# Performance work log

Measured on AMD Instinct MI355X. Metric: run time of the kernel, lower is better.

The kernel has to match this reference:

```python
import jax, jax.numpy as jnp
from jax import lax
import numpy as np

EPS = 1e-5

def sign_ste(x):
    # Binarize to {-1,+1} with straight-through estimator (matches BNN Binarize)
    return x + lax.stop_gradient(jnp.where(x >= 0, 1.0, -1.0).astype(x.dtype) - x)

def bn(x, g, b, m, v, axis):
    shp = [1] * x.ndim
    shp[axis] = -1
    inv = g.reshape(shp) / jnp.sqrt(v.reshape(shp) + EPS)
    return (x - m.reshape(shp)) * inv + b.reshape(shp)

def bconv(x, w, b, p):
    # binarized-weight conv, NCHW / OIHW
    y = lax.conv_general_dilated(x, sign_ste(w), (1, 1), [(p, p), (p, p)],
                                 dimension_numbers=('NCHW', 'OIHW', 'NCHW'))
    return y + b[None, :, None, None]

def conv_block(x, w, b, g, bt, m, v, p):
    # BinarizeConv2d -> BatchNorm2d(eval) -> Hardtanh -> Quantizer(1 bit)
    return sign_ste(jnp.clip(bn(bconv(x, w, b, p), g, bt, m, v, 1), -1.0, 1.0))

def maxpool2(x):
    return lax.reduce_window(x, -jnp.inf, lax.max, (1, 1, 2, 2), (1, 1, 2, 2), 'VALID')


def setup_inputs() -> dict:
    key = jax.random.key(0)
    ks = iter(jax.random.split(key, 64))
    B = 4096
    d = {}
    d['x'] = jax.random.normal(next(ks), (B, 1, 28, 28), dtype=jnp.float32)

    def u(shape):
        return jax.random.uniform(next(ks), shape, minval=-1.0, maxval=1.0, dtype=jnp.float32)

    def bn_params(c, pre):
        d[pre + 'g'] = u((c,)) * 0.5 + 1.0
        d[pre + 'bt'] = u((c,)) * 0.1
        d[pre + 'm'] = u((c,)) * 0.1
        d[pre + 'v'] = jax.random.uniform(next(ks), (c,), minval=0.5, maxval=1.5, dtype=jnp.float32)

    # stem conv 1->16, k=3
    d['w1'] = u((16, 1, 3, 3)); d['b1'] = jnp.full((16,), 0.01, jnp.float32); bn_params(16, '')
    d['g1'], d['bt1'], d['m1'], d['v1'] = d.pop('g'), d.pop('bt'), d.pop('m'), d.pop('v')
    # inception branches 16->32 each
    d['wa'] = u((32, 16, 1, 1)); d['ba'] = jnp.full((32,), 0.01, jnp.float32); bn_params(32, 'a_')
    d['wb'] = u((32, 16, 3, 3)); d['bb'] = jnp.full((32,), 0.01, jnp.float32); bn_params(32, 'b_')
    d['wc'] = u((32, 16, 5, 5)); d['bc'] = jnp.full((32,), 0.01, jnp.float32); bn_params(32, 'c_')
    # classifier
    d['wf1'] = u((1024, 7 * 7 * 3 * 32)); d['bf1'] = jnp.full((1024,), 0.01, jnp.float32); bn_params(1024, 'f1_')
    d['wf2'] = u((10, 1024)); d['bf2'] = jnp.full((10,), 0.01, jnp.float32); bn_params(10, 'f2_')
    return d


def reference(x, w1, b1, g1, bt1, m1, v1,
              wa, ba, a_g, a_bt, a_m, a_v,
              wb, bb, b_g, b_bt, b_m, b_v,
              wc, bc, c_g, c_bt, c_m, c_v,
              wf1, bf1, f1_g, f1_bt, f1_m, f1_v,
              wf2, bf2, f2_g, f2_bt, f2_m, f2_v):
    h = conv_block(x, w1, b1, g1, bt1, m1, v1, 1)          # [B,16,28,28]
    h = maxpool2(h)                                         # [B,16,14,14]
    h = sign_ste(h)  # BinarizeConv2d binarizes its input (>1 channel); no-op on +/-1
    ya = conv_block(h, wa, ba, a_g, a_bt, a_m, a_v, 0)
    yb = conv_block(h, wb, bb, b_g, b_bt, b_m, b_v, 1)
    yc = conv_block(h, wc, bc, c_g, c_bt, c_m, c_v, 2)
    h = jnp.concatenate([ya, yb, yc], axis=1)               # [B,96,14,14]
    h = maxpool2(h)                                         # [B,96,7,7]
    h = h.reshape(h.shape[0], -1)                           # [B,4704] (NCHW flatten)
    # fc1: binarized input + binarized weights, BN1d, hardtanh, quantize
    h = sign_ste(h) @ sign_ste(wf1).T + bf1
    h = sign_ste(jnp.clip(bn(h, f1_g, f1_bt, f1_m, f1_v, 1), -1.0, 1.0))
    # dropout is identity in eval mode
    h = sign_ste(h) @ sign_ste(wf2).T + bf2
    h = bn(h, f2_g, f2_bt, f2_m, f2_v, 1)
    return jax.nn.log_softmax(h, axis=-1)                   # [B,10]
```

## Files before the change

### kernel.cpp

```cpp
#include <hip/hip_runtime.h>
#include <stdint.h>

typedef unsigned long long u64;
typedef unsigned int u32;
typedef unsigned short u16;

struct InPtrs { const float* p[37]; };

#define OFF_THR1     0
#define OFF_W1D      128
#define OFF_WREC     1280
#define OFF_SMAXBC   4352
#define OFF_SMAXF1   11008
#define OFF_WF2P     15104
#define OFF_A2       16384
#define OFF_C2       16448
#define OFF_WF1P     16512
#define OFF_H2       622720
#define OFF_HB2      3047552

__device__ __forceinline__ int clampi(int v, int lo, int hi) { return v < lo ? lo : (v > hi ? hi : v); }

__global__ __launch_bounds__(1024) void kprep(InPtrs P, char* __restrict__ ws) {
  const float* w1 = P.p[1]; const float* b1 = P.p[2];
  const float* g1 = P.p[3]; const float* bt1 = P.p[4]; const float* m1 = P.p[5]; const float* v1 = P.p[6];
  const float* wa = P.p[7]; const float* ba = P.p[8];
  const float* ag = P.p[9]; const float* abt = P.p[10]; const float* am = P.p[11]; const float* av = P.p[12];
  const float* wb = P.p[13]; const float* bb = P.p[14];
  const float* bg = P.p[15]; const float* bbt = P.p[16]; const float* bm = P.p[17]; const float* bv = P.p[18];
  const float* wc = P.p[19]; const float* bc = P.p[20];
  const float* bf1 = P.p[26];
  const float* f1g = P.p[27]; const float* f1bt = P.p[28]; const float* f1m = P.p[29]; const float* f1v = P.p[30];
  const float* wf2 = P.p[31]; const float* bf2 = P.p[32];
  const float* cg = P.p[21]; const float* cbt = P.p[22]; const float* cm = P.p[23]; const float* cv = P.p[24];
  const float* f2g = P.p[33]; const float* f2bt = P.p[34]; const float* f2m = P.p[35]; const float* f2v = P.p[36];

  double* thr1 = (double*)(ws + OFF_THR1);
  double* w1d  = (double*)(ws + OFF_W1D);
  u64* wrec = (u64*)(ws + OFF_WREC);
  u64* smaxbc = (u64*)(ws + OFF_SMAXBC);
  int* smf1 = (int*)(ws + OFF_SMAXF1);
  u64* wf2p = (u64*)(ws + OFF_WF2P);
  float* a2 = (float*)(ws + OFF_A2);
  float* c2 = (float*)(ws + OFF_C2);

  __shared__ u64 wbpL[96];
  __shared__ u64 wcpL[256];
  __shared__ double thBL[32], thCL[32];
  __shared__ u32 wamS[32], smaS[32];

  int t = threadIdx.x;
  int wave = t >> 6, lane = t & 63;

  if (t < 144) w1d[t] = (w1[t] >= 0.f) ? 1.0 : -1.0;
  if (t < 16) {
    double inv = (double)g1[t] / sqrt((double)v1[t] + 1e-5);
    thr1[t] = (double)m1[t] - (double)bt1[t] / inv - (double)b1[t];
  }
  if (t < 32) {
    u32 m = 0;
    for (int c = 0; c < 16; c++) if (wa[t*16+c] >= 0.f) m |= 1u << c;
    wamS[t] = m;
    double ia = (double)ag[t] / sqrt((double)av[t] + 1e-5);
    double thA = (double)am[t] - (double)abt[t]/ia - (double)ba[t];
    int kmin = (int)ceil(thA);
    int sm = (16 - kmin) >> 1;
    smaS[t] = (u32)clampi(sm + 1, 0, 65535);
    double ib = (double)bg[t] / sqrt((double)bv[t] + 1e-5);
    thBL[t] = (double)bm[t] - (double)bbt[t]/ib - (double)bb[t];
    double ic = (double)cg[t] / sqrt((double)cv[t] + 1e-5);
    thCL[t] = (double)cm[t] - (double)cbt[t]/ic - (double)bc[t];
  }
  for (int w = wave; w < 96; w += 16) {
    int ch = w / 3, k = w - 3*ch;
    int tt = 4*k + (lane >> 4), c = lane & 15;
    bool pred = false;
    if (tt < 9) pred = (wb[ch*144 + c*9 + tt] >= 0.f);
    u64 m = __ballot(pred);
    if (lane == 0) wbpL[w] = m;
  }
  for (int w = wave; w < 256; w += 16) {
    int ch = w >> 3, k = w & 7;
    int tt = 4*k + (lane >> 4), c = lane & 15;
    bool pred = false;
    if (k < 7 && tt < 25) pred = (wc[ch*400 + c*25 + tt] >= 0.f);
    u64 m = __ballot(pred);
    if (lane == 0) wcpL[w] = m;
  }
  for (int w = wave; w < 160; w += 16) {
    int o = w >> 4, kk = w & 15;
    bool pred = (wf2[o*1024 + kk*64 + lane] >= 0.f);
    u64 m = __ballot(pred);
    if (lane == 0) wf2p[w] = m;
  }
  if (t < 10) {
    double inv = (double)f2g[t] / sqrt((double)f2v[t] + 1e-5);
    a2[t] = (float)inv;
    c2[t] = (float)(((double)bf2[t] - (double)f2m[t]) * inv + (double)f2bt[t]);
  }
  {
    int o = t;
    double inv = (double)f1g[o] / sqrt((double)f1v[o] + 1e-5);
    double th = (double)f1m[o] - (double)f1bt[o]/inv - (double)bf1[o];
    int kmin = (int)ceil(th);
    smf1[o] = ((4704 - kmin) >> 1) + 1;
  }
  __syncthreads();
  if (t < 384) {
    int ch = t / 12, k = t - 12*ch;
    u64 v = 0;
    if (k < 7) v = wcpL[ch*8 + k];
    else if (k < 10) v = wbpL[ch*3 + (k - 7)];
    wrec[ch*12 + k] = v;
  }
  if (t < 800) {
    const int irep[5] = {0, 1, 5, 12, 13};
    int cls = t >> 5, ch = t & 31;
    int rc = cls / 5, cc = cls - 5*rc;
    int ir = irep[rc], jr = irep[cc];
    u64 invC[7] = {0,0,0,0,0,0,0};
    u64 invB[3] = {0,0,0};
    int nInvC = 0, nInvB = 0;
    #pragma unroll
    for (int tt = 0; tt < 25; tt++) {
      int di = tt/5 - 2, dj = tt%5 - 2;
      bool val = (ir+di >= 0 && ir+di < 14 && jr+dj >= 0 && jr+dj < 14);
      if (!val) { invC[tt>>2] |= 0xFFFFull << ((tt&3)*16); nInvC++; }
    }
    #pragma unroll
    for (int tt = 0; tt < 9; tt++) {
      int di = tt/3 - 1, dj = tt%3 - 1;
      bool val = (ir+di >= 0 && ir+di < 14 && jr+dj >= 0 && jr+dj < 14);
      if (!val) { invB[tt>>2] |= 0xFFFFull << ((tt&3)*16); nInvB++; }
    }
    int pinvC = 0;
    #pragma unroll
    for (int k = 0; k < 7; k++) pinvC += __popcll(wcpL[ch*8+k] & invC[k]);
    int pinvB = 0;
    #pragma unroll
    for (int k = 0; k < 3; k++) pinvB += __popcll(wbpL[ch*3+k] & invB[k]);
    int nvC = 16*(25 - nInvC), nvB = 16*(9 - nInvB);
    int kminC = (int)ceil(thCL[ch]);
    int kminB = (int)ceil(thBL[ch]);
    int smC = ((nvC - kminC) >> 1) + pinvC;
    int smB = ((nvB - kminB) >> 1) + pinvB;
    u64 pB = (u64)clampi(smB + 1, 0, 65535);
    u64 pC = (u64)clampi(smC + 1, 0, 65535);
    smaxbc[cls*33 + ch] = ((u64)wamS[ch] << 48) | ((u64)smaS[ch] << 32) | (pB << 16) | pC;
  }
}

__global__ __launch_bounds__(256) void kfused(const float* __restrict__ x, const float* __restrict__ wf1,
                                              const char* __restrict__ ws,
                                              u32* __restrict__ h2u32, u64* __restrict__ wf1p) {
  __shared__ float wshF[144];
  __shared__ float thrF[16];
  __shared__ double thrD[16];
  __shared__ u16 hp[324];
  __shared__ u32 rr[196][3];
  __shared__ u64 smbc[825];
  __shared__ __align__(16) u64 wrecL[384];

  int t = threadIdx.x;

  if (blockIdx.x < 1024) {
    unsigned char* flag = (unsigned char*)smbc;
    int o = blockIdx.x;
    const float* row = wf1 + (size_t)o*4704;
    for (int i = t; i < 4704; i += 256) flag[i] = (row[i] >= 0.f);
    __syncthreads();
    int w0 = t >> 6, lane = t & 63;
    for (int w = w0; w < 74; w += 4) {
      int fp = w*64 + lane;
      bool bit = false;
      if (fp < 4704) { int s = fp / 96, c = fp - 96*s; bit = flag[c*49 + s] != 0; }
      u64 m = __ballot(bit);
      if (lane == 0) wf1p[(size_t)o*74 + w] = m;
    }
    return;
  }

  int b = blockIdx.x - 1024;
  const double* w1d  = (const double*)(ws + OFF_W1D);
  const double* thr1 = (const double*)(ws + OFF_THR1);
  const u64* wrec_g = (const u64*)(ws + OFF_WREC);
  const u64* smaxbc_g = (const u64*)(ws + OFF_SMAXBC);

  if (t < 144) wshF[t] = (float)w1d[t];
  else if (t < 160) { thrF[t-144] = (float)thr1[t-144]; thrD[t-144] = thr1[t-144]; }
  for (int i = t; i < 384; i += 256) wrecL[i] = wrec_g[i];
  for (int i = t; i < 825; i += 256) smbc[i] = smaxbc_g[i];
  {
    u32* hp32 = (u32*)hp;
    for (int i = t; i < 162; i += 256) hp32[i] = 0;
  }
  __syncthreads();

  int pi = t / 14, pj = t - 14*pi;
  if (t < 196) {
    const float* xi = x + (size_t)b*784;
    float p[16];
    #pragma unroll
    for (int r = 0; r < 4; r++) {
      int ii = 2*pi - 1 + r;
      #pragma unroll
      for (int c = 0; c < 4; c++) {
        int jj = 2*pj - 1 + c;
        bool v = (ii >= 0 && ii < 28 && jj >= 0 && jj < 28);
        int a = v ? (ii*28 + jj) : 0;
        float f = xi[a];
        p[r*4+c] = v ? f : 0.0f;
      }
    }
    u32 bits = 0;
    for (int o = 0; o < 16; o++) {
      float a00 = 0.f, a01 = 0.f, a10 = 0.f, a11 = 0.f;
      #pragma unroll
      for (int dy = 0; dy < 3; dy++)
        #pragma unroll
        for (int dx = 0; dx < 3; dx++) {
          float w = wshF[o*9 + dy*3 + dx];
          a00 += p[dy*4 + dx]       * w;
          a01 += p[dy*4 + dx + 1]   * w;
          a10 += p[(dy+1)*4 + dx]   * w;
          a11 += p[(dy+1)*4 + dx+1] * w;
        }
      float th = thrF[o];
      float mx = fmaxf(fmaxf(a00, a01), fmaxf(a10, a11));
      bool bit;
      if (fabsf(mx - th) < 5e-4f) {
        double d00 = 0.0, d01 = 0.0, d10 = 0.0, d11 = 0.0;
        #pragma unroll
        for (int dy = 0; dy < 3; dy++)
          #pragma unroll
          for (int dx = 0; dx < 3; dx++) {
            double w = (double)wshF[o*9 + dy*3 + dx];
            d00 += (double)p[dy*4 + dx]       * w;
            d01 += (double)p[dy*4 + dx + 1]   * w;
            d10 += (double)p[(dy+1)*4 + dx]   * w;
            d11 += (double)p[(dy+1)*4 + dx+1] * w;
          }
        double thd = thrD[o];
        bit = (d00 >= thd) || (d01 >= thd) || (d10 >= thd) || (d11 >= thd);
      } else {
        bit = (mx >= th);
      }
      bits |= (u32)bit << o;
    }
    hp[(pi+2)*18 + (pj+2)] = (u16)bits;
  }
  __syncthreads();

  if (t < 196) {
    const u16* hpb = &hp[pi*18 + pj];
    u32 tp[25];
    #pragma unroll
    for (int r = 0; r < 5; r++)
      #pragma unroll
      for (int c = 0; c < 5; c++) tp[r*5+c] = hpb[r*18 + c];
    u32 h0 = tp[12];
    u64 qc[6], qb[2];
    u32 qc6 = tp[24], qb2 = tp[18];
    qc[0] = (u64)tp[0]  | (u64)tp[1]<<16  | (u64)tp[2]<<32  | (u64)tp[3]<<48;
    qc[1] = (u64)tp[4]  | (u64)tp[5]<<16  | (u64)tp[6]<<32  | (u64)tp[7]<<48;
    qc[2] = (u64)tp[8]  | (u64)tp[9]<<16  | (u64)tp[10]<<32 | (u64)tp[11]<<48;
    qc[3] = (u64)tp[12] | (u64)tp[13]<<16 | (u64)tp[14]<<32 | (u64)tp[15]<<48;
    qc[4] = (u64)tp[16] | (u64)tp[17]<<16 | (u64)tp[18]<<32 | (u64)tp[19]<<48;
    qc[5] = (u64)tp[20] | (u64)tp[21]<<16 | (u64)tp[22]<<32 | (u64)tp[23]<<48;
    qb[0] = (u64)tp[6]  | (u64)tp[7]<<16  | (u64)tp[8]<<32  | (u64)tp[11]<<48;
    qb[1] = (u64)tp[12] | (u64)tp[13]<<16 | (u64)tp[16]<<32 | (u64)tp[17]<<48;
    int rc = (pi < 2) ? pi : (pi > 11 ? pi - 9 : 2);
    int cc = (pj < 2) ? pj : (pj > 11 ? pj - 9 : 2);
    const u64* mrow = &smbc[(rc*5 + cc)*33];
    const ulonglong2* R2 = (const ulonglong2*)wrecL;
    u32 r0 = 0, r1 = 0, r2 = 0;
    #pragma unroll 8
    for (int ch = 0; ch < 32; ch++) {
      ulonglong2 w01 = R2[ch*6+0], w23 = R2[ch*6+1], w45 = R2[ch*6+2];
      ulonglong2 w67 = R2[ch*6+3], w89 = R2[ch*6+4];
      u64 meta = mrow[ch];
      int Sc = __popcll(qc[0]^w01.x) + __popcll(qc[1]^w01.y) + __popcll(qc[2]^w23.x)
             + __popcll(qc[3]^w23.y) + __popcll(qc[4]^w45.x) + __popcll(qc[5]^w45.y)
             + __popc(qc6 ^ (u32)w67.x);
      int Sb = __popcll(qb[0]^w67.y) + __popcll(qb[1]^w89.x) + __popc(qb2 ^ (u32)w89.y);
      int Sa = __popc(h0 ^ (u32)(meta >> 48));
      r0 |= (u32)(Sa < (int)((meta >> 32) & 0xFFFFu)) << ch;
      r1 |= (u32)(Sb < (int)((meta >> 16) & 0xFFFFu)) << ch;
      r2 |= (u32)(Sc < (int)(meta & 0xFFFFu)) << ch;
    }
    rr[t][0] = r0; rr[t][1] = r1; rr[t][2] = r2;
  }
  __syncthreads();
  if (t < 148) {
    u32 v = 0;
    if (t < 147) {
      int s = t / 3, qq = t - 3*s;
      int sp = s / 7, sj = s - 7*sp;
      int base = (2*sp)*14 + 2*sj;
      v = rr[base][qq] | rr[base+1][qq] | rr[base+14][qq] | rr[base+15][qq];
    }
    h2u32[(size_t)b*148 + t] = v;
  }
}

__global__ __launch_bounds__(256) void kfc1(const u64* __restrict__ h2, const u64* __restrict__ wf1p,
                                            const int* __restrict__ smf1, u64* __restrict__ hb2) {
  __shared__ __align__(16) u64 aL[64*74];
  __shared__ __align__(16) u64 wL[64*74];
  __shared__ unsigned char bitsb[64][64];
  int bx = blockIdx.x, by = blockIdx.y, t = threadIdx.x;
  const ulonglong2* ga = reinterpret_cast<const ulonglong2*>(h2 + (size_t)by*(64*74));
  ulonglong2* la = reinterpret_cast<ulonglong2*>(aL);
  for (int i = t; i < 64*37; i += 256) la[i] = ga[i];
  const ulonglong2* gw = reinterpret_cast<const ulonglong2*>(wf1p + (size_t)bx*(64*74));
  ulonglong2* lw = reinterpret_cast<ulonglong2*>(wL);
  for (int i = t; i < 64*37; i += 256) {
    int o = i / 37, w2 = i - 37*o;
    int po = ((o & 15) << 2) | (o >> 4);
    lw[po*37 + w2] = gw[i];
  }
  __syncthreads();
  int ig = t & 15, og = t >> 4;
  const ulonglong2* A0 = reinterpret_cast<const ulonglong2*>(aL + (ig     )*74);
  const ulonglong2* A1 = reinterpret_cast<const ulonglong2*>(aL + (ig + 16)*74);
  const ulonglong2* A2 = reinterpret_cast<const ulonglong2*>(aL + (ig + 32)*74);
  const ulonglong2* A3 = reinterpret_cast<const ulonglong2*>(aL + (ig + 48)*74);
  const ulonglong2* W0 = reinterpret_cast<const ulonglong2*>(wL + (og*4 + 0)*74);
  const ulonglong2* W1 = reinterpret_cast<const ulonglong2*>(wL + (og*4 + 1)*74);
  const ulonglong2* W2 = reinterpret_cast<const ulonglong2*>(wL + (og*4 + 2)*74);
  const ulonglong2* W3 = reinterpret_cast<const ulonglong2*>(wL + (og*4 + 3)*74);
  int s[4][4];
  #pragma unroll
  for (int i = 0; i < 4; i++)
    #pragma unroll
    for (int j = 0; j < 4; j++) s[i][j] = 0;
  for (int w = 0; w < 37; w++) {
    ulonglong2 b0 = W0[w], b1 = W1[w], b2 = W2[w], b3 = W3[w];
    ulonglong2 a;
    a = A0[w];
    s[0][0] += __popcll(a.x^b0.x)+__popcll(a.y^b0.y); s[0][1] += __popcll(a.x^b1.x)+__popcll(a.y^b1.y);
    s[0][2] += __popcll(a.x^b2.x)+__popcll(a.y^b2.y); s[0][3] += __popcll(a.x^b3.x)+__popcll(a.y^b3.y);
    a = A1[w];
    s[1][0] += __popcll(a.x^b0.x)+__popcll(a.y^b0.y); s[1][1] += __popcll(a.x^b1.x)+__popcll(a.y^b1.y);
    s[1][2] += __popcll(a.x^b2.x)+__popcll(a.y^b2.y); s[1][3] += __popcll(a.x^b3.x)+__popcll(a.y^b3.y);
    a = A2[w];
    s[2][0] += __popcll(a.x^b0.x)+__popcll(a.y^b0.y); s[2][1] += __popcll(a.x^b1.x)+__popcll(a.y^b1.y);
    s[2][2] += __popcll(a.x^b2.x)+__popcll(a.y^b2.y); s[2][3] += __popcll(a.x^b3.x)+__popcll(a.y^b3.y);
    a = A3[w];
    s[3][0] += __popcll(a.x^b0.x)+__popcll(a.y^b0.y); s[3][1] += __popcll(a.x^b1.x)+__popcll(a.y^b1.y);
    s[3][2] += __popcll(a.x^b2.x)+__popcll(a.y^b2.y); s[3][3] += __popcll(a.x^b3.x)+__popcll(a.y^b3.y);
  }
  int th0 = smf1[bx*64 + og];
  int th1 = smf1[bx*64 + og + 16];
  int th2 = smf1[bx*64 + og + 32];
  int th3 = smf1[bx*64 + og + 48];
  #pragma unroll
  for (int i = 0; i < 4; i++) {
    int im = ig + 16*i;
    bitsb[im][og     ] = s[i][0] < th0;
    bitsb[im][og + 16] = s[i][1] < th1;
    bitsb[im][og + 32] = s[i][2] < th2;
    bitsb[im][og + 48] = s[i][3] < th3;
  }
  __syncthreads();
  if (t < 64) {
    u64 wd = 0;
    #pragma unroll
    for (int j = 0; j < 64; j++) wd |= (u64)bitsb[t][j] << j;
    hb2[(size_t)(by*64 + t)*16 + bx] = wd;
  }
}

__global__ __launch_bounds__(256) void kfc2(const u64* __restrict__ hb2, const char* __restrict__ ws,
                                            float* __restrict__ out, int B) {
  __shared__ u64 w2[160];
  __shared__ float a2s[10], c2s[10];
  const u64* wf2p = (const u64*)(ws + OFF_WF2P);
  const float* a2 = (const float*)(ws + OFF_A2);
  const float* c2 = (const float*)(ws + OFF_C2);
  int t = threadIdx.x;
  for (int i = t; i < 160; i += 256) w2[i] = wf2p[i];
  if (t < 10) { a2s[t] = a2[t]; c2s[t] = c2[t]; }
  __syncthreads();
  int img = blockIdx.x*256 + t;
  if (img >= B) return;
  u64 a[16];
  #pragma unroll
  for (int w = 0; w < 16; w++) a[w] = hb2[(size_t)img*16 + w];
  float z[10];
  #pragma unroll
  for (int o = 0; o < 10; o++) {
    int S = 0;
    #pragma unroll
    for (int w = 0; w < 16; w++) S += __popcll(a[w] ^ w2[o*16 + w]);
    z[o] = (float)(1024 - 2*S) * a2s[o] + c2s[o];
  }
  float M = z[0];
  #pragma unroll
  for (int o = 1; o < 10; o++) M = fmaxf(M, z[o]);
  float se = 0.f;
  #pragma unroll
  for (int o = 0; o < 10; o++) se += expf(z[o] - M);
  float lse = M + logf(se);
  #pragma unroll
  for (int o = 0; o < 10; o++) out[(size_t)img*10 + o] = z[o] - lse;
}

extern "C" void kernel_launch(void* const* d_in, const int* in_sizes, int n_in,
                              void* d_out, int out_size, void* d_ws, size_t ws_size,
                              hipStream_t stream) {
  int B = in_sizes[0] / 784;
  char* ws = (char*)d_ws;
  InPtrs P;
  for (int i = 0; i < 37; i++) P.p[i] = (const float*)d_in[i];

  kprep<<<1, 1024, 0, stream>>>(P, ws);
  kfused<<<1024 + B, 256, 0, stream>>>((const float*)d_in[0], (const float*)d_in[25], ws,
                                       (u32*)(ws + OFF_H2), (u64*)(ws + OFF_WF1P));
  dim3 g(16, B/64);
  kfc1<<<g, 256, 0, stream>>>((const u64*)(ws + OFF_H2), (const u64*)(ws + OFF_WF1P),
                              (const int*)(ws + OFF_SMAXF1), (u64*)(ws + OFF_HB2));
  kfc2<<<(B + 255)/256, 256, 0, stream>>>((const u64*)(ws + OFF_HB2), ws, (float*)d_out, B);
}
```

Measured before the change: 144.0 us.

## Transpose fc1 activations to feature-major layout and read directly from global

The conv kernel now stores the pooled binary activations transposed, with each 128-bit feature chunk laid out contiguously across images. The fc1 kernel drops its LDS staging of activations and loads them straight from global memory with coalesced 16-byte reads per chunk. This frees LDS and removes a load phase and part of the barrier wait, which could raise occupancy. In exchange, every activation word is read from global or L2 four times across the output-group threads, and the kfused stores become strided by B.

```diff
diff --git a/kernel.cpp b/kernel.cpp
--- a/kernel.cpp
+++ b/kernel.cpp
@@ -152,7 +152,7 @@
 
 __global__ __launch_bounds__(256) void kfused(const float* __restrict__ x, const float* __restrict__ wf1,
                                               const char* __restrict__ ws,
-                                              u32* __restrict__ h2u32, u64* __restrict__ wf1p) {
+                                              u32* __restrict__ h2t, u64* __restrict__ wf1p, int B) {
   __shared__ float wshF[144];
   __shared__ float thrF[16];
   __shared__ double thrD[16];
@@ -299,19 +299,15 @@
       int base = (2*sp)*14 + 2*sj;
       v = rr[base][qq] | rr[base+1][qq] | rr[base+14][qq] | rr[base+15][qq];
     }
-    h2u32[(size_t)b*148 + t] = v;
+    h2t[((size_t)(t >> 2)*B + b)*4 + (t & 3)] = v;
   }
 }
 
-__global__ __launch_bounds__(256) void kfc1(const u64* __restrict__ h2, const u64* __restrict__ wf1p,
-                                            const int* __restrict__ smf1, u64* __restrict__ hb2) {
-  __shared__ __align__(16) u64 aL[64*74];
+__global__ __launch_bounds__(256) void kfc1(const ulonglong2* __restrict__ h2t, const u64* __restrict__ wf1p,
+                                            const int* __restrict__ smf1, u64* __restrict__ hb2, int B) {
   __shared__ __align__(16) u64 wL[64*74];
   __shared__ unsigned char bitsb[64][64];
   int bx = blockIdx.x, by = blockIdx.y, t = threadIdx.x;
-  const ulonglong2* ga = reinterpret_cast<const ulonglong2*>(h2 + (size_t)by*(64*74));
-  ulonglong2* la = reinterpret_cast<ulonglong2*>(aL);
-  for (int i = t; i < 64*37; i += 256) la[i] = ga[i];
   const ulonglong2* gw = reinterpret_cast<const ulonglong2*>(wf1p + (size_t)bx*(64*74));
   ulonglong2* lw = reinterpret_cast<ulonglong2*>(wL);
   for (int i = t; i < 64*37; i += 256) {
@@ -321,10 +317,7 @@
   }
   __syncthreads();
   int ig = t & 15, og = t >> 4;
-  const ulonglong2* A0 = reinterpret_cast<const ulonglong2*>(aL + (ig     )*74);
-  const ulonglong2* A1 = reinterpret_cast<const ulonglong2*>(aL + (ig + 16)*74);
-  const ulonglong2* A2 = reinterpret_cast<const ulonglong2*>(aL + (ig + 32)*74);
-  const ulonglong2* A3 = reinterpret_cast<const ulonglong2*>(aL + (ig + 48)*74);
+  int im0 = by*64 + ig;
   const ulonglong2* W0 = reinterpret_cast<const ulonglong2*>(wL + (og*4 + 0)*74);
   const ulonglong2* W1 = reinterpret_cast<const ulonglong2*>(wL + (og*4 + 1)*74);
   const ulonglong2* W2 = reinterpret_cast<const ulonglong2*>(wL + (og*4 + 2)*74);
@@ -334,19 +327,20 @@
   for (int i = 0; i < 4; i++)
     #pragma unroll
     for (int j = 0; j < 4; j++) s[i][j] = 0;
-  for (int w = 0; w < 37; w++) {
-    ulonglong2 b0 = W0[w], b1 = W1[w], b2 = W2[w], b3 = W3[w];
+  for (int p = 0; p < 37; p++) {
+    const ulonglong2* Ap = h2t + (size_t)p*B + im0;
+    ulonglong2 b0 = W0[p], b1 = W1[p], b2 = W2[p], b3 = W3[p];
     ulonglong2 a;
-    a = A0[w];
+    a = Ap[0];
     s[0][0] += __popcll(a.x^b0.x)+__popcll(a.y^b0.y); s[0][1] += __popcll(a.x^b1.x)+__popcll(a.y^b1.y);
     s[0][2] += __popcll(a.x^b2.x)+__popcll(a.y^b2.y); s[0][3] += __popcll(a.x^b3.x)+__popcll(a.y^b3.y);
-    a = A1[w];
+    a = Ap[16];
     s[1][0] += __popcll(a.x^b0.x)+__popcll(a.y^b0.y); s[1][1] += __popcll(a.x^b1.x)+__popcll(a.y^b1.y);
     s[1][2] += __popcll(a.x^b2.x)+__popcll(a.y^b2.y); s[1][3] += __popcll(a.x^b3.x)+__popcll(a.y^b3.y);
-    a = A2[w];
+    a = Ap[32];
     s[2][0] += __popcll(a.x^b0.x)+__popcll(a.y^b0.y); s[2][1] += __popcll(a.x^b1.x)+__popcll(a.y^b1.y);
     s[2][2] += __popcll(a.x^b2.x)+__popcll(a.y^b2.y); s[2][3] += __popcll(a.x^b3.x)+__popcll(a.y^b3.y);
-    a = A3[w];
+    a = Ap[48];
     s[3][0] += __popcll(a.x^b0.x)+__popcll(a.y^b0.y); s[3][1] += __popcll(a.x^b1.x)+__popcll(a.y^b1.y);
     s[3][2] += __popcll(a.x^b2.x)+__popcll(a.y^b2.y); s[3][3] += __popcll(a.x^b3.x)+__popcll(a.y^b3.y);
   }
@@ -416,9 +410,9 @@
 
   kprep<<<1, 1024, 0, stream>>>(P, ws);
   kfused<<<1024 + B, 256, 0, stream>>>((const float*)d_in[0], (const float*)d_in[25], ws,
-                                       (u32*)(ws + OFF_H2), (u64*)(ws + OFF_WF1P));
+                                       (u32*)(ws + OFF_H2), (u64*)(ws + OFF_WF1P), B);
   dim3 g(16, B/64);
-  kfc1<<<g, 256, 0, stream>>>((const u64*)(ws + OFF_H2), (const u64*)(ws + OFF_WF1P),
-                              (const int*)(ws + OFF_SMAXF1), (u64*)(ws + OFF_HB2));
+  kfc1<<<g, 256, 0, stream>>>((const ulonglong2*)(ws + OFF_H2), (const u64*)(ws + OFF_WF1P),
+                              (const int*)(ws + OFF_SMAXF1), (u64*)(ws + OFF_HB2), B);
   kfc2<<<(B + 255)/256, 256, 0, stream>>>((const u64*)(ws + OFF_HB2), ws, (float*)d_out, B);
 }
```

New measurement: 147.4 us. 2.4% more time.
